# Kernel tuning notes

Measured on AMD Instinct MI355X. Metric: run time of the kernel, lower is better.

The kernel has to match this reference:

```python
import jax, jax.numpy as jnp
import numpy as np

B, S, D, H = 2, 2048, 1024, 16
DK = D // H


def setup_inputs() -> dict:
    key = jax.random.key(0)
    ks = jax.random.split(key, 11)
    inp = {
        'query': jax.random.normal(ks[0], (B, S, D), jnp.float32),
        'key':   jax.random.normal(ks[1], (B, S, D), jnp.float32),
        'value': jax.random.normal(ks[2], (B, S, D), jnp.float32),
        # causal mask, broadcast over heads like mask.unsqueeze(1)
        'mask': jnp.broadcast_to(jnp.tril(jnp.ones((S, S), jnp.int32)), (B, S, S)),
    }
    s = 1.0 / np.sqrt(D)
    for i, nm in enumerate(['q', 'k', 'v', 'o']):
        inp[f'W{nm}'] = jax.random.normal(ks[3 + i], (D, D), jnp.float32) * s
        inp[f'b{nm}'] = jnp.zeros((D,), jnp.float32)
    return inp


def reference(query, key, value, mask, Wq, bq, Wk, bk, Wv, bv, Wo, bo):
    def proj(x, W, b):
        # [B,S,D] -> [B,H,S,DK]
        y = x @ W.T + b
        return y.reshape(B, S, H, DK).transpose(0, 2, 1, 3)

    q = proj(query, Wq, bq)
    k = proj(key, Wk, bk)
    v = proj(value, Wv, bv)

    scores = jnp.einsum('bhsd,bhtd->bhst', q, k) / np.sqrt(DK)
    scores = jnp.where(mask[:, None, :, :] == 0, -1e9, scores)
    p = jax.nn.softmax(scores, axis=-1)  # dropout in eval mode = identity
    x = jnp.einsum('bhst,bhtd->bhsd', p, v)
    x = x.transpose(0, 2, 1, 3).reshape(B, S, D)
    return x @ Wo.T + bo
```

## Files before the change

kernel.cpp:

```cpp
#include <hip/hip_runtime.h>
#include <stdint.h>

#define BB 2
#define SS 2048
#define DD 1024
#define HH 16
#define DKK 64
#define EE 4194304
#define WEE 1048576
#define QSCALE 0.1803368801f

typedef __attribute__((ext_vector_type(8))) short bf16x8;
typedef __attribute__((ext_vector_type(4))) float f32x4;
typedef __attribute__((ext_vector_type(4))) unsigned short u16x4;

__device__ __forceinline__ unsigned short f2bf(float f) {
    union { float f; unsigned int i; } c; c.f = f;
    unsigned int u = c.i;
    return (unsigned short)((u + 0x7FFFu + ((u >> 16) & 1u)) >> 16);
}
__device__ __forceinline__ float bf2f(unsigned short u) {
    union { float f; unsigned int i; } c; c.i = ((unsigned int)u) << 16; return c.f;
}
__device__ __forceinline__ float load1f(const void* p, int idx, int isbf) {
    return isbf ? bf2f(((const unsigned short*)p)[idx]) : ((const float*)p)[idx];
}

#define GLDS16(gp, lp)                                                              \
    __builtin_amdgcn_global_load_lds(                                               \
        (const __attribute__((address_space(1))) void*)(gp),                        \
        (__attribute__((address_space(3))) void*)(lp), 16, 0, 0)

__global__ void detect_dtype_k(const unsigned short* __restrict__ q,
                               int* __restrict__ flag) {
    const int lane = threadIdx.x;
    unsigned short u = q[lane * 2];
    int ex = (u >> 7) & 0xFF;
    bool bad = (ex != 0) && (ex < 110 || ex > 137);
    unsigned long long m = __ballot(bad);
    if (lane == 0) *flag = (__popcll(m) >= 8) ? 0 : 1;
}

__global__ __launch_bounds__(256)
void convert_k(const float* __restrict__ q, const float* __restrict__ k,
               const float* __restrict__ v,
               const float* __restrict__ wq, const float* __restrict__ wk,
               const float* __restrict__ wv, const float* __restrict__ wo,
               unsigned short* __restrict__ Xc, unsigned short* __restrict__ Wc,
               const int* __restrict__ flagp)
{
    if (*flagp) return;
    const size_t e = ((size_t)blockIdx.x * 256 + threadIdx.x) * 8;
    const float* src; unsigned short* dst; size_t off;
    if (e < (size_t)3 * EE) {
        const int t = (int)(e / EE);
        src = (t == 0) ? q : (t == 1) ? k : v;
        off = e - (size_t)t * EE;
        dst = Xc + (size_t)t * EE;
    } else {
        const size_t we = e - (size_t)3 * EE;
        const int t = (int)(we >> 20);
        src = (t == 0) ? wq : (t == 1) ? wk : (t == 2) ? wv : wo;
        off = we & (WEE - 1);
        dst = Wc + (size_t)t * WEE;
    }
    const float4 a = *(const float4*)(src + off);
    const float4 b = *(const float4*)(src + off + 4);
    bf16x8 o;
    o[0] = (short)f2bf(a.x); o[1] = (short)f2bf(a.y);
    o[2] = (short)f2bf(a.z); o[3] = (short)f2bf(a.w);
    o[4] = (short)f2bf(b.x); o[5] = (short)f2bf(b.y);
    o[6] = (short)f2bf(b.z); o[7] = (short)f2bf(b.w);
    *(bf16x8*)(dst + off) = o;
}

__global__ __launch_bounds__(256)
void gemm_qkv(const void* __restrict__ Xq, const void* __restrict__ Xk,
              const void* __restrict__ Xv,
              const void* __restrict__ Wqp, const void* __restrict__ Wkp,
              const void* __restrict__ Wvp,
              const void* __restrict__ bqp, const void* __restrict__ bkp,
              const void* __restrict__ bvp,
              const unsigned short* __restrict__ Xc,
              const unsigned short* __restrict__ Wc,
              unsigned short* __restrict__ qb, unsigned short* __restrict__ kb,
              unsigned short* __restrict__ vtb, const int* __restrict__ flagp)
{
    const int isbf = *flagp;
    const int z = blockIdx.z;
    const unsigned short* Xg = isbf
        ? (const unsigned short*)((z == 0) ? Xq : (z == 1) ? Xk : Xv)
        : Xc + (size_t)z * EE;
    const unsigned short* Wg = isbf
        ? (const unsigned short*)((z == 0) ? Wqp : (z == 1) ? Wkp : Wvp)
        : Wc + (size_t)z * WEE;
    const void* bias = (z == 0) ? bqp : (z == 1) ? bkp : bvp;

    __shared__ __align__(16) unsigned short As[3][128 * 32];
    __shared__ __align__(16) unsigned short Bs[3][128 * 32];

    const int tid  = threadIdx.x;
    const int lane = tid & 63, w = tid >> 6;
    const int l15  = lane & 15, quad = lane >> 4;
    const int wr = (w >> 1) * 64, wc = (w & 1) * 64;
    const int r0 = blockIdx.x * 128, c0 = blockIdx.y * 128;
    const int srow = tid >> 2;
    const int scol = (((tid & 3) ^ ((tid >> 3) & 3)) << 3);
    const int rdo  = ((quad ^ ((l15 >> 1) & 3)) << 3);

    const unsigned short* xp0 = Xg + (size_t)(r0 + srow) * DD + scol;
    const unsigned short* xp1 = Xg + (size_t)(r0 + 64 + srow) * DD + scol;
    const unsigned short* wp0 = Wg + (size_t)(c0 + srow) * DD + scol;
    const unsigned short* wp1 = Wg + (size_t)(c0 + 64 + srow) * DD + scol;

#define STAGE_G(buf, kk)                                                       \
    do {                                                                       \
        GLDS16(xp0 + (kk), &As[buf][tid * 8]);                                 \
        GLDS16(xp1 + (kk), &As[buf][2048 + tid * 8]);                          \
        GLDS16(wp0 + (kk), &Bs[buf][tid * 8]);                                 \
        GLDS16(wp1 + (kk), &Bs[buf][2048 + tid * 8]);                          \
    } while (0)

#define LOADFRAG_G(buf)                                                        \
    do {                                                                       \
        _Pragma("unroll")                                                      \
        for (int mi = 0; mi < 4; ++mi)                                         \
            af[mi] = *(const bf16x8*)(&As[buf][(wr + mi * 16 + l15) * 32 +     \
                                               rdo]);                          \
        _Pragma("unroll")                                                      \
        for (int ni = 0; ni < 4; ++ni)                                         \
            bfr[ni] = *(const bf16x8*)(&Bs[buf][(wc + ni * 16 + l15) * 32 +    \
                                                rdo]);                         \
    } while (0)

#define MFMA_G()                                                               \
    do {                                                                       \
        __builtin_amdgcn_s_setprio(1);                                         \
        _Pragma("unroll")                                                      \
        for (int mi = 0; mi < 4; ++mi)                                         \
            _Pragma("unroll")                                                  \
            for (int ni = 0; ni < 4; ++ni)                                     \
                acc[mi][ni] = __builtin_amdgcn_mfma_f32_16x16x32_bf16(         \
                    af[mi], bfr[ni], acc[mi][ni], 0, 0, 0);                    \
        __builtin_amdgcn_s_setprio(0);                                         \
    } while (0)

#define PHASE_G(cb, nb, kn)                                                    \
    do {                                                                       \
        asm volatile("s_waitcnt vmcnt(4)" ::: "memory");                       \
        __builtin_amdgcn_s_barrier();                                          \
        __builtin_amdgcn_sched_barrier(0);                                     \
        LOADFRAG_G(cb);                                                        \
        STAGE_G(nb, kn);                                                       \
        __builtin_amdgcn_sched_barrier(0);                                     \
        MFMA_G();                                                              \
    } while (0)

    f32x4 acc[4][4] = {};
    bf16x8 af[4], bfr[4];

    STAGE_G(0, 0);
    STAGE_G(1, 32);
    for (int s = 0; s < 30; s += 3) {
        const int k0 = s * 32;
        PHASE_G(0, 2, k0 + 64);
        PHASE_G(1, 0, k0 + 96);
        PHASE_G(2, 1, k0 + 128);
    }
    asm volatile("s_waitcnt vmcnt(4)" ::: "memory");
    __builtin_amdgcn_s_barrier();
    __builtin_amdgcn_sched_barrier(0);
    LOADFRAG_G(0);
    MFMA_G();
    asm volatile("s_waitcnt vmcnt(0)" ::: "memory");
    __builtin_amdgcn_s_barrier();
    __builtin_amdgcn_sched_barrier(0);
    LOADFRAG_G(1);
    MFMA_G();

#pragma unroll
    for (int mi = 0; mi < 4; ++mi) {
#pragma unroll
        for (int ni = 0; ni < 4; ++ni) {
            const int col = c0 + wc + ni * 16 + l15;
            const float bv = load1f(bias, col, isbf);
            const int h = col >> 6, dk = col & 63;
            const int m0 = r0 + wr + mi * 16 + quad * 4;
            const int bb = m0 >> 11, s0 = m0 & (SS - 1);
            const int bh = bb * HH + h;
            if (z == 0) {
#pragma unroll
                for (int r = 0; r < 4; ++r)
                    qb[((size_t)bh * SS + s0 + r) * DKK + dk] =
                        f2bf((acc[mi][ni][r] + bv) * QSCALE);
            } else if (z == 1) {
#pragma unroll
                for (int r = 0; r < 4; ++r) {
                    const int t = s0 + r;
                    kb[((((size_t)bh * 128 + (t >> 4)) * 8 + (dk >> 3)) * 16 +
                        (t & 15)) * 8 + (dk & 7)] = f2bf(acc[mi][ni][r] + bv);
                }
            } else {
                u16x4 pv;
#pragma unroll
                for (int r = 0; r < 4; ++r) pv[r] = f2bf(acc[mi][ni][r] + bv);
                const int t = s0;
                *(u16x4*)&vtb[((((size_t)bh * 64 + (t >> 5)) * 4 + (dk >> 4)) * 64 +
                               ((t >> 3) & 3) * 16 + (dk & 15)) * 8 + (t & 7)] = pv;
            }
        }
    }
#undef STAGE_G
#undef LOADFRAG_G
#undef MFMA_G
#undef PHASE_G
}

template <bool MASKED>
__device__ __forceinline__ void attn_tile_lds(
    const int t0, const int q0, const int l15, const int quad,
    const unsigned short* Kl, const unsigned short* Vl,
    const bf16x8 (&qf)[2], f32x4 (&Oa)[4], float (&ls)[4],
    unsigned short* __restrict__ Pw)
{
    bf16x8 kf[4][2];
#pragma unroll
    for (int ni = 0; ni < 4; ++ni)
#pragma unroll
        for (int ks = 0; ks < 2; ++ks)
            kf[ni][ks] = *(const bf16x8*)(Kl +
                (((ni * 8 + ks * 4 + quad) * 16 + l15) * 8));

    f32x4 sc[4] = {};
    __builtin_amdgcn_s_setprio(1);
#pragma unroll
    for (int ks = 0; ks < 2; ++ks)
#pragma unroll
        for (int ni = 0; ni < 4; ++ni)
            sc[ni] = __builtin_amdgcn_mfma_f32_16x16x32_bf16(
                qf[ks], kf[ni][ks], sc[ni], 0, 0, 0);
    __builtin_amdgcn_s_setprio(0);

    bf16x8 vf[4][2];
#pragma unroll
    for (int nd = 0; nd < 4; ++nd)
#pragma unroll
        for (int ks = 0; ks < 2; ++ks)
            vf[nd][ks] = *(const bf16x8*)(Vl +
                (((ks * 4 + nd) * 64 + quad * 16 + l15) * 8));

#pragma unroll
    for (int ni = 0; ni < 4; ++ni)
#pragma unroll
        for (int r = 0; r < 4; ++r) {
            float s = sc[ni][r];
            if (MASKED && (t0 + ni * 16 + l15 > q0 + quad * 4 + r))
                s = -__builtin_inff();
            const float p = __builtin_amdgcn_exp2f(s);
            const unsigned int pu = __float_as_uint(p);
            ls[r] += __uint_as_float(pu & 0xFFFF0000u);
            Pw[(quad * 4 + r) * 72 + ni * 16 + l15] = (unsigned short)(pu >> 16);
        }

    bf16x8 pf[2];
#pragma unroll
    for (int ks = 0; ks < 2; ++ks)
        pf[ks] = *(const bf16x8*)(Pw + l15 * 72 + ks * 32 + quad * 8);
    __builtin_amdgcn_s_setprio(1);
#pragma unroll
    for (int ks = 0; ks < 2; ++ks)
#pragma unroll
        for (int nd = 0; nd < 4; ++nd)
            Oa[nd] = __builtin_amdgcn_mfma_f32_16x16x32_bf16(
                pf[ks], vf[nd][ks], Oa[nd], 0, 0, 0);
    __builtin_amdgcn_s_setprio(0);
}

__global__ __launch_bounds__(256)
void attn_mfma(const unsigned short* __restrict__ Qg,
               const unsigned short* __restrict__ Kf,
               const unsigned short* __restrict__ Vf,
               unsigned short* __restrict__ Og)
{
    __shared__ __align__(16) unsigned short Ks[2][4096];
    __shared__ __align__(16) unsigned short Vs[2][4096];
    __shared__ __align__(16) unsigned short Ps[4][16 * 72];
    const int tid  = threadIdx.x;
    const int lane = tid & 63, w = tid >> 6;
    const int l15 = lane & 15, quad = lane >> 4;
    const int bh = blockIdx.x;
    const int g = gridDim.y - 1 - blockIdx.y;
    const int qt = g * 4 + w;
    const int q0 = qt * 16;
    unsigned short* Pw = &Ps[w][0];

    const unsigned short* Qb = Qg + (size_t)bh * SS * DKK;
    const unsigned short* Kb = Kf + (size_t)bh * SS * DKK;
    const unsigned short* Vb = Vf + (size_t)bh * SS * DKK;

#define STAGE_T(buf, tt)                                                       \
    do {                                                                       \
        GLDS16(Kb + (size_t)(tt) * 4096 + tid * 8,        &Ks[buf][tid * 8]);  \
        GLDS16(Kb + (size_t)(tt) * 4096 + 2048 + tid * 8, &Ks[buf][2048 + tid * 8]); \
        GLDS16(Vb + (size_t)(tt) * 4096 + tid * 8,        &Vs[buf][tid * 8]);  \
        GLDS16(Vb + (size_t)(tt) * 4096 + 2048 + tid * 8, &Vs[buf][2048 + tid * 8]); \
    } while (0)

    bf16x8 qf[2];
#pragma unroll
    for (int ks = 0; ks < 2; ++ks)
        qf[ks] = *(const bf16x8*)(Qb + (size_t)(q0 + l15) * DKK + ks * 32 + quad * 8);

    f32x4 Oa[4] = {};
    float ls[4] = {};

    STAGE_T(0, 0);
    int cur = 0;
    for (int tt = 0; tt < g; ++tt) {
        STAGE_T(cur ^ 1, tt + 1);
        asm volatile("s_waitcnt vmcnt(4)" ::: "memory");
        __builtin_amdgcn_s_barrier();
        __builtin_amdgcn_sched_barrier(0);
        attn_tile_lds<false>(tt * 64, q0, l15, quad,
                             &Ks[cur][0], &Vs[cur][0], qf, Oa, ls, Pw);
        __builtin_amdgcn_s_barrier();
        cur ^= 1;
    }
    asm volatile("s_waitcnt vmcnt(0)" ::: "memory");
    __builtin_amdgcn_s_barrier();
    __builtin_amdgcn_sched_barrier(0);
    attn_tile_lds<true>(g * 64, q0, l15, quad,
                        &Ks[cur][0], &Vs[cur][0], qf, Oa, ls, Pw);
#undef STAGE_T

    const int bb = bh >> 4, h = bh & (HH - 1);
#pragma unroll
    for (int r = 0; r < 4; ++r) {
        float l = ls[r];
        l += __shfl_xor(l, 1);
        l += __shfl_xor(l, 2);
        l += __shfl_xor(l, 4);
        l += __shfl_xor(l, 8);
        const float inv = 1.0f / l;
        const int s = q0 + quad * 4 + r;
#pragma unroll
        for (int nd = 0; nd < 4; ++nd)
            Og[((size_t)bb * SS + s) * DD + h * 64 + nd * 16 + l15] =
                f2bf(Oa[nd][r] * inv);
    }
}

__global__ __launch_bounds__(256)
void gemm_out(const unsigned short* __restrict__ Xa, const void* __restrict__ W,
              const unsigned short* __restrict__ Wcs,
              const void* __restrict__ bias, void* __restrict__ Y,
              const int* __restrict__ flagp)
{
    const int isbf = *flagp;
    const unsigned short* Wg = isbf ? (const unsigned short*)W : Wcs;

    __shared__ __align__(16) unsigned short As[3][64 * 32];
    __shared__ __align__(16) unsigned short Bs[3][128 * 32];

    const int tid  = threadIdx.x;
    const int lane = tid & 63, w = tid >> 6;
    const int l15  = lane & 15, quad = lane >> 4;
    const int wr = (w >> 1) * 32, wc = (w & 1) * 64;
    const int r0 = blockIdx.x * 64, c0 = blockIdx.y * 128;
    const int srow = tid >> 2;
    const int scol = (((tid & 3) ^ ((tid >> 3) & 3)) << 3);
    const int rdo  = ((quad ^ ((l15 >> 1) & 3)) << 3);

    const unsigned short* xp0 = Xa + (size_t)(r0 + srow) * DD + scol;
    const unsigned short* wp0 = Wg + (size_t)(c0 + srow) * DD + scol;
    const unsigned short* wp1 = Wg + (size_t)(c0 + 64 + srow) * DD + scol;

#define STAGE_O(buf, kk)                                                       \
    do {                                                                       \
        GLDS16(xp0 + (kk), &As[buf][tid * 8]);                                 \
        GLDS16(wp0 + (kk), &Bs[buf][tid * 8]);                                 \
        GLDS16(wp1 + (kk), &Bs[buf][2048 + tid * 8]);                          \
    } while (0)

#define LOADFRAG_O(buf)                                                        \
    do {                                                                       \
        _Pragma("unroll")                                                      \
        for (int mi = 0; mi < 2; ++mi)                                         \
            af[mi] = *(const bf16x8*)(&As[buf][(wr + mi * 16 + l15) * 32 +     \
                                               rdo]);                          \
        _Pragma("unroll")                                                      \
        for (int ni = 0; ni < 4; ++ni)                                         \
            bfr[ni] = *(const bf16x8*)(&Bs[buf][(wc + ni * 16 + l15) * 32 +    \
                                                rdo]);                         \
    } while (0)

#define MFMA_O()                                                               \
    do {                                                                       \
        __builtin_amdgcn_s_setprio(1);                                         \
        _Pragma("unroll")                                                      \
        for (int mi = 0; mi < 2; ++mi)                                         \
            _Pragma("unroll")                                                  \
            for (int ni = 0; ni < 4; ++ni)                                     \
                acc[mi][ni] = __builtin_amdgcn_mfma_f32_16x16x32_bf16(         \
                    af[mi], bfr[ni], acc[mi][ni], 0, 0, 0);                    \
        __builtin_amdgcn_s_setprio(0);                                         \
    } while (0)

#define PHASE_O(cb, nb, kn)                                                    \
    do {                                                                       \
        asm volatile("s_waitcnt vmcnt(3)" ::: "memory");                       \
        __builtin_amdgcn_s_barrier();                                          \
        __builtin_amdgcn_sched_barrier(0);                                     \
        LOADFRAG_O(cb);                                                        \
        STAGE_O(nb, kn);                                                       \
        __builtin_amdgcn_sched_barrier(0);                                     \
        MFMA_O();                                                              \
    } while (0)

    f32x4 acc[2][4] = {};
    bf16x8 af[2], bfr[4];

    STAGE_O(0, 0);
    STAGE_O(1, 32);
    for (int s = 0; s < 30; s += 3) {
        const int k0 = s * 32;
        PHASE_O(0, 2, k0 + 64);
        PHASE_O(1, 0, k0 + 96);
        PHASE_O(2, 1, k0 + 128);
    }
    asm volatile("s_waitcnt vmcnt(3)" ::: "memory");
    __builtin_amdgcn_s_barrier();
    __builtin_amdgcn_sched_barrier(0);
    LOADFRAG_O(0);
    MFMA_O();
    asm volatile("s_waitcnt vmcnt(0)" ::: "memory");
    __builtin_amdgcn_s_barrier();
    __builtin_amdgcn_sched_barrier(0);
    LOADFRAG_O(1);
    MFMA_O();

#pragma unroll
    for (int mi = 0; mi < 2; ++mi) {
#pragma unroll
        for (int ni = 0; ni < 4; ++ni) {
            const int col = c0 + wc + ni * 16 + l15;
            const float bv = load1f(bias, col, isbf);
            const int m0 = r0 + wr + mi * 16 + quad * 4;
#pragma unroll
            for (int r = 0; r < 4; ++r) {
                const float val = acc[mi][ni][r] + bv;
                if (isbf) ((unsigned short*)Y)[(size_t)(m0 + r) * DD + col] = f2bf(val);
                else      ((float*)Y)[(size_t)(m0 + r) * DD + col] = val;
            }
        }
    }
#undef STAGE_O
#undef LOADFRAG_O
#undef MFMA_O
#undef PHASE_O
}

extern "C" void kernel_launch(void* const* d_in, const int* in_sizes, int n_in,
                              void* d_out, int out_size, void* d_ws, size_t ws_size,
                              hipStream_t stream)
{
    const void* query = d_in[0];
    const void* key   = d_in[1];
    const void* value = d_in[2];
    const void* Wq = d_in[4];  const void* bq = d_in[5];
    const void* Wk = d_in[6];  const void* bk = d_in[7];
    const void* Wv = d_in[8];  const void* bv = d_in[9];
    const void* Wo = d_in[10]; const void* bo = d_in[11];

    int* flag = (int*)d_ws;
    unsigned short* base = (unsigned short*)((char*)d_ws + 256);
    const size_t E = EE;
    unsigned short* qb  = base;
    unsigned short* kb  = base + E;
    unsigned short* vtb = base + 2 * E;
    unsigned short* Wc  = base + 3 * E;
    unsigned short* Xc  = base + 4 * E;
    unsigned short* ab  = Xc;

    detect_dtype_k<<<1, 64, 0, stream>>>((const unsigned short*)query, flag);
    convert_k<<<8192, 256, 0, stream>>>((const float*)query, (const float*)key,
                                        (const float*)value, (const float*)Wq,
                                        (const float*)Wk, (const float*)Wv,
                                        (const float*)Wo, Xc, Wc, flag);
    gemm_qkv<<<dim3(32, 8, 3), 256, 0, stream>>>(query, key, value, Wq, Wk, Wv,
                                                 bq, bk, bv, Xc, Wc,
                                                 qb, kb, vtb, flag);
    attn_mfma<<<dim3(32, 32), 256, 0, stream>>>(qb, kb, vtb, ab);
    gemm_out<<<dim3(64, 8), 256, 0, stream>>>(ab, Wo, Wc + 3 * (size_t)WEE, bo,
                                              d_out, flag);
}
```

Baseline: 231.3 us.

## Use 512-thread attention blocks covering 128 query rows with interleaved causal ordering

The attention kernel now runs 8 waves per block, so each block covers 128 query rows and shares each staged K/V tile among twice as many waves. The grid halves in y, and block order alternates long and short causal workloads to balance the load. Each thread stages one 16-byte K and V chunk per tile instead of two. Within a block, waves whose query rows finish earlier sit idle while the others process the last tile, and the larger block may reduce occupancy.

```diff
diff --git a/kernel.cpp b/kernel.cpp
--- a/kernel.cpp
+++ b/kernel.cpp
@@ -276,7 +276,7 @@
     __builtin_amdgcn_s_setprio(0);
 }
 
-__global__ __launch_bounds__(256)
+__global__ __launch_bounds__(512)
 void attn_mfma(const unsigned short* __restrict__ Qg,
                const unsigned short* __restrict__ Kf,
                const unsigned short* __restrict__ Vf,
@@ -284,28 +284,23 @@
 {
     __shared__ __align__(16) unsigned short Ks[2][4096];
     __shared__ __align__(16) unsigned short Vs[2][4096];
-    __shared__ __align__(16) unsigned short Ps[4][16 * 72];
+    __shared__ __align__(16) unsigned short Ps[8][16 * 72];
     const int tid  = threadIdx.x;
     const int lane = tid & 63, w = tid >> 6;
     const int l15 = lane & 15, quad = lane >> 4;
     const int bh = blockIdx.x;
-    const int g = gridDim.y - 1 - blockIdx.y;
-    const int qt = g * 4 + w;
+    const int by = blockIdx.y;
+    const int g = (by < 8) ? (15 - 2 * by) : (2 * (by - 8));
+    const int qt = g * 8 + w;
     const int q0 = qt * 16;
+    const int nf = 2 * g + (w >> 2);
+    const int NTT = 2 * g + 2;
     unsigned short* Pw = &Ps[w][0];
 
     const unsigned short* Qb = Qg + (size_t)bh * SS * DKK;
     const unsigned short* Kb = Kf + (size_t)bh * SS * DKK;
     const unsigned short* Vb = Vf + (size_t)bh * SS * DKK;
 
-#define STAGE_T(buf, tt)                                                       \
-    do {                                                                       \
-        GLDS16(Kb + (size_t)(tt) * 4096 + tid * 8,        &Ks[buf][tid * 8]);  \
-        GLDS16(Kb + (size_t)(tt) * 4096 + 2048 + tid * 8, &Ks[buf][2048 + tid * 8]); \
-        GLDS16(Vb + (size_t)(tt) * 4096 + tid * 8,        &Vs[buf][tid * 8]);  \
-        GLDS16(Vb + (size_t)(tt) * 4096 + 2048 + tid * 8, &Vs[buf][2048 + tid * 8]); \
-    } while (0)
-
     bf16x8 qf[2];
 #pragma unroll
     for (int ks = 0; ks < 2; ++ks)
@@ -314,24 +309,28 @@
     f32x4 Oa[4] = {};
     float ls[4] = {};
 
-    STAGE_T(0, 0);
-    int cur = 0;
-    for (int tt = 0; tt < g; ++tt) {
-        STAGE_T(cur ^ 1, tt + 1);
-        asm volatile("s_waitcnt vmcnt(4)" ::: "memory");
+    GLDS16(Kb + tid * 8, &Ks[0][tid * 8]);
+    GLDS16(Vb + tid * 8, &Vs[0][tid * 8]);
+
+    for (int tt = 0; tt < NTT; ++tt) {
+        const int cur = tt & 1;
+        if (tt + 1 < NTT) {
+            GLDS16(Kb + (size_t)(tt + 1) * 4096 + tid * 8, &Ks[cur ^ 1][tid * 8]);
+            GLDS16(Vb + (size_t)(tt + 1) * 4096 + tid * 8, &Vs[cur ^ 1][tid * 8]);
+            asm volatile("s_waitcnt vmcnt(2)" ::: "memory");
+        } else {
+            asm volatile("s_waitcnt vmcnt(0)" ::: "memory");
+        }
         __builtin_amdgcn_s_barrier();
         __builtin_amdgcn_sched_barrier(0);
-        attn_tile_lds<false>(tt * 64, q0, l15, quad,
-                             &Ks[cur][0], &Vs[cur][0], qf, Oa, ls, Pw);
+        if (tt < nf)
+            attn_tile_lds<false>(tt * 64, q0, l15, quad,
+                                 &Ks[cur][0], &Vs[cur][0], qf, Oa, ls, Pw);
+        else if (tt == nf)
+            attn_tile_lds<true>(tt * 64, q0, l15, quad,
+                                &Ks[cur][0], &Vs[cur][0], qf, Oa, ls, Pw);
         __builtin_amdgcn_s_barrier();
-        cur ^= 1;
-    }
-    asm volatile("s_waitcnt vmcnt(0)" ::: "memory");
-    __builtin_amdgcn_s_barrier();
-    __builtin_amdgcn_sched_barrier(0);
-    attn_tile_lds<true>(g * 64, q0, l15, quad,
-                        &Ks[cur][0], &Vs[cur][0], qf, Oa, ls, Pw);
-#undef STAGE_T
+    }
 
     const int bb = bh >> 4, h = bh & (HH - 1);
 #pragma unroll
@@ -490,7 +489,7 @@
     gemm_qkv<<<dim3(32, 8, 3), 256, 0, stream>>>(query, key, value, Wq, Wk, Wv,
                                                  bq, bk, bv, Xc, Wc,
                                                  qb, kb, vtb, flag);
-    attn_mfma<<<dim3(32, 32), 256, 0, stream>>>(qb, kb, vtb, ab);
+    attn_mfma<<<dim3(32, 16), 512, 0, stream>>>(qb, kb, vtb, ab);
     gemm_out<<<dim3(64, 8), 256, 0, stream>>>(ab, Wo, Wc + 3 * (size_t)WEE, bo,
                                               d_out, flag);
 }
```

After: 237.5 us. 1.03x slower.
